# Performance work log

Measured on AMD Instinct MI355X. Metric: run time of the kernel, lower is better.

Reference implementation:

```python
import jax, jax.numpy as jnp
import numpy as np
from jax.experimental import sparse as jsparse

N_ITEMS = 20000   # item catalog size (S is [N_ITEMS, N_ITEMS])
N_USERS = 2048    # user batch
NNZ = 4_000_000


def setup_inputs() -> dict:
    key = jax.random.key(0)
    k1, k2, k3, k4 = jax.random.split(key, 4)
    X = jax.random.normal(k1, (N_USERS, N_ITEMS), dtype=jnp.float32)
    S_vals = jax.random.normal(k2, (NNZ,), dtype=jnp.float32)
    S_rows = jax.random.randint(k3, (NNZ,), 0, N_ITEMS, dtype=jnp.int32)
    S_cols = jax.random.randint(k4, (NNZ,), 0, N_ITEMS, dtype=jnp.int32)
    return {"X": X, "S_vals": S_vals, "S_rows": S_rows, "S_cols": S_cols}


def reference(X, S_vals, S_rows, S_cols):
    # torch.sparse.mm(S, X.t()).t()  ==  X @ S^T, with S sparse COO.
    indices = jnp.stack([S_rows, S_cols], axis=1)  # [nnz, 2]
    S = jsparse.BCOO((S_vals, indices), shape=(N_ITEMS, N_ITEMS))
    # (S @ X^T)^T -> [n_users, n_items]; duplicate indices sum, matching COO semantics.
    return (S @ X.T).T
```

## Files before the change

kernel.cpp:

```cpp
#include <hip/hip_runtime.h>

#define N_ITEMS 20000
#define N_USERS 2048
#define NNZ     4000000
#define LDP     2112
#define HALF_ITEMS 10000
#define CAP_H   192

typedef float    f32x4 __attribute__((ext_vector_type(4)));
typedef unsigned u32x4 __attribute__((ext_vector_type(4)));

#define OFF_XT     ((size_t)0)
#define OFF_CSRPK  ((size_t)84480000)
#define OFF_CNT    (OFF_CSRPK + 30720000)

static __device__ __forceinline__ unsigned short f2bf(float f) {
  unsigned u = __float_as_uint(f);
  unsigned r = (u + 0x7fffu + ((u >> 16) & 1u)) >> 16;
  return (unsigned short)r;
}

#define NT_BLOCKS (313 * 32)
#define NS_BLOCKS ((NNZ / 4 + 255) / 256)

__global__ __launch_bounds__(256) void prep_kernel(
    const float* __restrict__ X, const float* __restrict__ vals,
    const int* __restrict__ rows, const int* __restrict__ cols,
    unsigned short* __restrict__ XT, int* __restrict__ cnt,
    unsigned* __restrict__ csr_pk) {
  int b = blockIdx.x;
  if (b < NT_BLOCKS) {
    __shared__ float tile[64][65];
    int k0 = (b % 313) * 64;
    int u0 = (b / 313) * 64;
    int lane = threadIdx.x & 63;
    int dq = threadIdx.x >> 6;
    #pragma unroll
    for (int m = 0; m < 16; ++m) {
      int u = u0 + dq + 4 * m;
      int k = k0 + lane;
      float v = 0.f;
      if (k < N_ITEMS) v = X[(size_t)u * N_ITEMS + k];
      tile[lane][dq + 4 * m] = v;
    }
    __syncthreads();
    #pragma unroll
    for (int m = 0; m < 16; ++m) {
      int k = k0 + dq + 4 * m;
      if (k < N_ITEMS)
        XT[(size_t)k * LDP + u0 + lane] = f2bf(tile[dq + 4 * m][lane]);
    }
  } else {
    int i = ((b - NT_BLOCKS) * 256 + threadIdx.x) * 4;
    if (i < NNZ) {
      int4   r4 = *reinterpret_cast<const int4*>(rows + i);
      int4   c4 = *reinterpret_cast<const int4*>(cols + i);
      float4 v4 = *reinterpret_cast<const float4*>(vals + i);
      #pragma unroll
      for (int k = 0; k < 4; ++k) {
        int   r = (k == 0) ? r4.x : (k == 1) ? r4.y : (k == 2) ? r4.z : r4.w;
        int   c = (k == 0) ? c4.x : (k == 1) ? c4.y : (k == 2) ? c4.z : c4.w;
        float v = (k == 0) ? v4.x : (k == 1) ? v4.y : (k == 2) ? v4.z : v4.w;
        int h = (c >= HALF_ITEMS) ? 1 : 0;
        int bin = 2 * r + h;
        int pos = atomicAdd(&cnt[bin], 1);
        if (pos >= CAP_H) pos = CAP_H - 1;
        csr_pk[bin * CAP_H + pos] =
            ((unsigned)(c - h * HALF_ITEMS) << 16) | (unsigned)f2bf(v);
      }
    }
  }
}

__global__ __launch_bounds__(256) void spmm_kernel(
    const int* __restrict__ cnt, const unsigned* __restrict__ csr_pk,
    const unsigned short* __restrict__ xt, float* __restrict__ out,
    int uc, int h) {
  __shared__ float tile[8][132];
  int wg = blockIdx.x;
  int xcd = wg & 7;
  int rb = wg >> 3;
  int u0 = (xcd * 2 + uc) * 128;
  int r0 = rb * 8;
  int lane = threadIdx.x & 63;
  int wave = __builtin_amdgcn_readfirstlane((int)(threadIdx.x >> 6));
  unsigned lane4 = 4 * (unsigned)lane;
  const char* xtb = (const char*)(xt + (size_t)h * HALF_ITEMS * LDP + u0);
  int ul = threadIdx.x >> 1;
  int rhalf = (threadIdx.x & 1) * 4;
  float* op = out + (size_t)(u0 + ul) * N_ITEMS + r0 + rhalf;

#define LOAD8(E, BASE)                                                       \
  { u32x4 q0 = __builtin_nontemporal_load(                                   \
        reinterpret_cast<const u32x4*>(csr_pk + (BASE)));                    \
    u32x4 q1 = __builtin_nontemporal_load(                                   \
        reinterpret_cast<const u32x4*>(csr_pk + (BASE) + 4));                \
    E[0] = q0.x; E[1] = q0.y; E[2] = q0.z; E[3] = q0.w;                      \
    E[4] = q1.x; E[5] = q1.y; E[6] = q1.z; E[7] = q1.w; }
#define GATHER8(G, E)                                                        \
  { _Pragma("unroll")                                                        \
    for (int k = 0; k < 8; ++k)                                              \
      G[k] = *reinterpret_cast<const unsigned*>(                             \
          xtb + ((E[k] >> 16) * (unsigned)(LDP * 2) + lane4)); }
#define FMA8(G, E)                                                           \
  { _Pragma("unroll")                                                        \
    for (int k = 0; k < 8; ++k) {                                            \
      float v  = __uint_as_float(E[k] << 16);                \
      float xl = __uint_as_float(G[k] << 16);                                \
      float xh = __uint_as_float(G[k]);                 \
      if (k & 1) { a2 = fmaf(v, xl, a2); a3 = fmaf(v, xh, a3); }             \
      else       { a0 = fmaf(v, xl, a0); a1 = fmaf(v, xh, a1); }             \
    } }

  if (h) {
    f32x4 i0 = __builtin_nontemporal_load(reinterpret_cast<const f32x4*>(op));
    tile[rhalf + 0][ul] = i0.x; tile[rhalf + 1][ul] = i0.y;
    tile[rhalf + 2][ul] = i0.z; tile[rhalf + 3][ul] = i0.w;
    __syncthreads();
  }

  #pragma unroll 1
  for (int rr = 0; rr < 2; ++rr) {
    int r = r0 + wave * 2 + rr;
    int bin = 2 * r + h;
    int jb = bin * CAP_H;
    int cr = __builtin_amdgcn_readfirstlane(cnt[bin]);
    if (cr > CAP_H) cr = CAP_H;
    int nb = (cr + 7) >> 3;
    float a0 = 0.f, a1 = 0.f, a2 = 0.f, a3 = 0.f;
    if (h) {
      a0 = tile[wave * 2 + rr][2 * lane];
      a1 = tile[wave * 2 + rr][2 * lane + 1];
    }
    if (nb >= 2) {
      unsigned e0[8], e1[8], g0[8], g1[8];
      LOAD8(e0, jb)
      GATHER8(g0, e0)
      LOAD8(e1, jb + 8)
      int b = 0;
      for (; b + 3 < nb; b += 2) {
        GATHER8(g1, e1)
        FMA8(g0, e0)
        LOAD8(e0, jb + (b + 2) * 8)
        GATHER8(g0, e0)
        FMA8(g1, e1)
        LOAD8(e1, jb + (b + 3) * 8)
      }
      GATHER8(g1, e1)
      FMA8(g0, e0)
      if (nb - b == 3) {
        LOAD8(e0, jb + (b + 2) * 8)
        GATHER8(g0, e0)
        FMA8(g1, e1)
        FMA8(g0, e0)
      } else {
        FMA8(g1, e1)
      }
    } else if (nb == 1) {
      unsigned e0[8], g0[8];
      LOAD8(e0, jb)
      GATHER8(g0, e0)
      FMA8(g0, e0)
    }
    tile[wave * 2 + rr][2 * lane]     = a0 + a2;
    tile[wave * 2 + rr][2 * lane + 1] = a1 + a3;
  }
#undef LOAD8
#undef GATHER8
#undef FMA8

  __syncthreads();
  f32x4 o;
  o.x = tile[rhalf + 0][ul]; o.y = tile[rhalf + 1][ul];
  o.z = tile[rhalf + 2][ul]; o.w = tile[rhalf + 3][ul];
  __builtin_nontemporal_store(o, reinterpret_cast<f32x4*>(op));
}

extern "C" void kernel_launch(void* const* d_in, const int* in_sizes, int n_in,
                              void* d_out, int out_size, void* d_ws, size_t ws_size,
                              hipStream_t stream) {
  const float* X      = (const float*)d_in[0];
  const float* S_vals = (const float*)d_in[1];
  const int*   S_rows = (const int*)d_in[2];
  const int*   S_cols = (const int*)d_in[3];
  float* out = (float*)d_out;

  char* ws = (char*)d_ws;
  unsigned short* XT = (unsigned short*)(ws + OFF_XT);
  unsigned* csr_pk   = (unsigned*)(ws + OFF_CSRPK);
  int* cnt           = (int*)(ws + OFF_CNT);

  hipMemsetAsync(cnt, 0, 2 * N_ITEMS * sizeof(int), stream);
  hipMemsetAsync(csr_pk, 0, (size_t)2 * N_ITEMS * CAP_H * sizeof(unsigned), stream);
  prep_kernel<<<NT_BLOCKS + NS_BLOCKS, 256, 0, stream>>>(
      X, S_vals, S_rows, S_cols, XT, cnt, csr_pk);
  for (int p = 0; p < 4; ++p)
    spmm_kernel<<<2500 * 8, 256, 0, stream>>>(cnt, csr_pk, XT, out,
                                              p >> 1, p & 1);
}
```

Baseline: 1.088 ms.

## Split columns into quarters and widen each lane to four users per gather

The column space is now split into four quarter-bins of 5000 items (capacity 128 each) instead of two halves. Each spmm launch covers all 256 users of an XCD slice, with every lane gathering 8 bytes (four bf16 users) and using packed two-wide FMAs, so one set of CSR entries is reused across twice as many users. Partial sums are accumulated into the output at the final store rather than preloaded into shared memory. Transpose and scatter are split into separate kernels, and the scatter no longer vectorises four entries per thread. The trade-offs are a tighter per-bin capacity, where overflowing entries get clamped into the last slot, and a larger memset of the padded CSR buffer.

Measured after the change: 2.754 ms. +153.0%, slower.

```diff
diff --git a/kernel.cpp b/kernel.cpp
--- a/kernel.cpp
+++ b/kernel.cpp
@@ -4,15 +4,17 @@
 #define N_USERS 2048
 #define NNZ     4000000
 #define LDP     2112
-#define HALF_ITEMS 10000
-#define CAP_H   192
+#define QITEMS  5000
+#define CAP_Q   128
 
 typedef float    f32x4 __attribute__((ext_vector_type(4)));
+typedef float    f32x2 __attribute__((ext_vector_type(2)));
 typedef unsigned u32x4 __attribute__((ext_vector_type(4)));
+typedef unsigned u32x2 __attribute__((ext_vector_type(2)));
 
 #define OFF_XT     ((size_t)0)
 #define OFF_CSRPK  ((size_t)84480000)
-#define OFF_CNT    (OFF_CSRPK + 30720000)
+#define OFF_CNT    (OFF_CSRPK + 40960000)
 
 static __device__ __forceinline__ unsigned short f2bf(float f) {
   unsigned u = __float_as_uint(f);
@@ -20,75 +22,59 @@
   return (unsigned short)r;
 }
 
-#define NT_BLOCKS (313 * 32)
-#define NS_BLOCKS ((NNZ / 4 + 255) / 256)
+__global__ __launch_bounds__(256) void transpose_kernel(
+    const float* __restrict__ X, unsigned short* __restrict__ XT) {
+  __shared__ float tile[64][65];
+  int k0 = blockIdx.x * 64;
+  int u0 = blockIdx.y * 64;
+  int lane = threadIdx.x & 63;
+  int dq = threadIdx.x >> 6;
+  #pragma unroll
+  for (int m = 0; m < 16; ++m) {
+    int u = u0 + dq + 4 * m;
+    int k = k0 + lane;
+    float v = 0.f;
+    if (k < N_ITEMS) v = X[(size_t)u * N_ITEMS + k];
+    tile[lane][dq + 4 * m] = v;
+  }
+  __syncthreads();
+  #pragma unroll
+  for (int m = 0; m < 16; ++m) {
+    int k = k0 + dq + 4 * m;
+    if (k < N_ITEMS)
+      XT[(size_t)k * LDP + u0 + lane] = f2bf(tile[dq + 4 * m][lane]);
+  }
+}
 
-__global__ __launch_bounds__(256) void prep_kernel(
-    const float* __restrict__ X, const float* __restrict__ vals,
+__global__ __launch_bounds__(256) void scatter_kernel(
     const int* __restrict__ rows, const int* __restrict__ cols,
-    unsigned short* __restrict__ XT, int* __restrict__ cnt,
+    const float* __restrict__ vals, int* __restrict__ cnt,
     unsigned* __restrict__ csr_pk) {
-  int b = blockIdx.x;
-  if (b < NT_BLOCKS) {
-    __shared__ float tile[64][65];
-    int k0 = (b % 313) * 64;
-    int u0 = (b / 313) * 64;
-    int lane = threadIdx.x & 63;
-    int dq = threadIdx.x >> 6;
-    #pragma unroll
-    for (int m = 0; m < 16; ++m) {
-      int u = u0 + dq + 4 * m;
-      int k = k0 + lane;
-      float v = 0.f;
-      if (k < N_ITEMS) v = X[(size_t)u * N_ITEMS + k];
-      tile[lane][dq + 4 * m] = v;
-    }
-    __syncthreads();
-    #pragma unroll
-    for (int m = 0; m < 16; ++m) {
-      int k = k0 + dq + 4 * m;
-      if (k < N_ITEMS)
-        XT[(size_t)k * LDP + u0 + lane] = f2bf(tile[dq + 4 * m][lane]);
-    }
-  } else {
-    int i = ((b - NT_BLOCKS) * 256 + threadIdx.x) * 4;
-    if (i < NNZ) {
-      int4   r4 = *reinterpret_cast<const int4*>(rows + i);
-      int4   c4 = *reinterpret_cast<const int4*>(cols + i);
-      float4 v4 = *reinterpret_cast<const float4*>(vals + i);
-      #pragma unroll
-      for (int k = 0; k < 4; ++k) {
-        int   r = (k == 0) ? r4.x : (k == 1) ? r4.y : (k == 2) ? r4.z : r4.w;
-        int   c = (k == 0) ? c4.x : (k == 1) ? c4.y : (k == 2) ? c4.z : c4.w;
-        float v = (k == 0) ? v4.x : (k == 1) ? v4.y : (k == 2) ? v4.z : v4.w;
-        int h = (c >= HALF_ITEMS) ? 1 : 0;
-        int bin = 2 * r + h;
-        int pos = atomicAdd(&cnt[bin], 1);
-        if (pos >= CAP_H) pos = CAP_H - 1;
-        csr_pk[bin * CAP_H + pos] =
-            ((unsigned)(c - h * HALF_ITEMS) << 16) | (unsigned)f2bf(v);
-      }
-    }
-  }
+  int i = blockIdx.x * 256 + threadIdx.x;
+  int r = rows[i];
+  int c = cols[i];
+  float v = vals[i];
+  int q = c / QITEMS;
+  int cl = c - q * QITEMS;
+  int bin = (r << 2) + q;
+  int pos = atomicAdd(&cnt[bin], 1);
+  if (pos >= CAP_Q) pos = CAP_Q - 1;
+  csr_pk[(bin << 7) + pos] = ((unsigned)cl << 16) | (unsigned)f2bf(v);
 }
 
 __global__ __launch_bounds__(256) void spmm_kernel(
     const int* __restrict__ cnt, const unsigned* __restrict__ csr_pk,
-    const unsigned short* __restrict__ xt, float* __restrict__ out,
-    int uc, int h) {
-  __shared__ float tile[8][132];
+    const unsigned short* __restrict__ xt, float* __restrict__ out, int q) {
+  __shared__ float tile[8][260];
   int wg = blockIdx.x;
   int xcd = wg & 7;
   int rb = wg >> 3;
-  int u0 = (xcd * 2 + uc) * 128;
+  int u0 = xcd * 256;
   int r0 = rb * 8;
   int lane = threadIdx.x & 63;
   int wave = __builtin_amdgcn_readfirstlane((int)(threadIdx.x >> 6));
-  unsigned lane4 = 4 * (unsigned)lane;
-  const char* xtb = (const char*)(xt + (size_t)h * HALF_ITEMS * LDP + u0);
-  int ul = threadIdx.x >> 1;
-  int rhalf = (threadIdx.x & 1) * 4;
-  float* op = out + (size_t)(u0 + ul) * N_ITEMS + r0 + rhalf;
+  unsigned lane8 = 8 * (unsigned)lane;
+  const char* xtb = (const char*)(xt + u0) + (size_t)q * QITEMS * (LDP * 2);
 
 #define LOAD8(E, BASE)                                                       \
   { u32x4 q0 = __builtin_nontemporal_load(                                   \
@@ -100,40 +86,35 @@
 #define GATHER8(G, E)                                                        \
   { _Pragma("unroll")                                                        \
     for (int k = 0; k < 8; ++k)                                              \
-      G[k] = *reinterpret_cast<const unsigned*>(                             \
-          xtb + ((E[k] >> 16) * (unsigned)(LDP * 2) + lane4)); }
+      G[k] = *reinterpret_cast<const u32x2*>(                                \
+          xtb + ((E[k] >> 16) * (unsigned)(LDP * 2) + lane8)); }
 #define FMA8(G, E)                                                           \
   { _Pragma("unroll")                                                        \
     for (int k = 0; k < 8; ++k) {                                            \
-      float v  = __uint_as_float(E[k] << 16);                \
-      float xl = __uint_as_float(G[k] << 16);                                \
-      float xh = __uint_as_float(G[k]);                 \
-      if (k & 1) { a2 = fmaf(v, xl, a2); a3 = fmaf(v, xh, a3); }             \
-      else       { a0 = fmaf(v, xl, a0); a1 = fmaf(v, xh, a1); }             \
+      float vv = __uint_as_float(E[k] << 16);                \
+      f32x2 v2; v2.x = vv; v2.y = vv;                                        \
+      f32x2 x01, x23;                                                        \
+      x01.x = __uint_as_float(G[k].x << 16);                                 \
+      x01.y = __uint_as_float(G[k].x);                  \
+      x23.x = __uint_as_float(G[k].y << 16);                                 \
+      x23.y = __uint_as_float(G[k].y);                  \
+      a01 = __builtin_elementwise_fma(v2, x01, a01);                         \
+      a23 = __builtin_elementwise_fma(v2, x23, a23);                         \
     } }
-
-  if (h) {
-    f32x4 i0 = __builtin_nontemporal_load(reinterpret_cast<const f32x4*>(op));
-    tile[rhalf + 0][ul] = i0.x; tile[rhalf + 1][ul] = i0.y;
-    tile[rhalf + 2][ul] = i0.z; tile[rhalf + 3][ul] = i0.w;
-    __syncthreads();
-  }
 
   #pragma unroll 1
   for (int rr = 0; rr < 2; ++rr) {
     int r = r0 + wave * 2 + rr;
-    int bin = 2 * r + h;
-    int jb = bin * CAP_H;
+    int bin = (r << 2) + q;
+    int jb = bin << 7;
     int cr = __builtin_amdgcn_readfirstlane(cnt[bin]);
-    if (cr > CAP_H) cr = CAP_H;
+    if (cr > CAP_Q) cr = CAP_Q;
     int nb = (cr + 7) >> 3;
-    float a0 = 0.f, a1 = 0.f, a2 = 0.f, a3 = 0.f;
-    if (h) {
-      a0 = tile[wave * 2 + rr][2 * lane];
-      a1 = tile[wave * 2 + rr][2 * lane + 1];
-    }
+    f32x2 a01, a23;
+    a01.x = 0.f; a01.y = 0.f; a23.x = 0.f; a23.y = 0.f;
     if (nb >= 2) {
-      unsigned e0[8], e1[8], g0[8], g1[8];
+      unsigned e0[8], e1[8];
+      u32x2 g0[8], g1[8];
       LOAD8(e0, jb)
       GATHER8(g0, e0)
       LOAD8(e1, jb + 8)
@@ -157,23 +138,34 @@
         FMA8(g1, e1)
       }
     } else if (nb == 1) {
-      unsigned e0[8], g0[8];
+      unsigned e0[8];
+      u32x2 g0[8];
       LOAD8(e0, jb)
       GATHER8(g0, e0)
       FMA8(g0, e0)
     }
-    tile[wave * 2 + rr][2 * lane]     = a0 + a2;
-    tile[wave * 2 + rr][2 * lane + 1] = a1 + a3;
+    f32x4 o;
+    o.x = a01.x; o.y = a01.y; o.z = a23.x; o.w = a23.y;
+    *reinterpret_cast<f32x4*>(&tile[wave * 2 + rr][4 * lane]) = o;
   }
 #undef LOAD8
 #undef GATHER8
 #undef FMA8
 
   __syncthreads();
-  f32x4 o;
-  o.x = tile[rhalf + 0][ul]; o.y = tile[rhalf + 1][ul];
-  o.z = tile[rhalf + 2][ul]; o.w = tile[rhalf + 3][ul];
-  __builtin_nontemporal_store(o, reinterpret_cast<f32x4*>(op));
+  int t = threadIdx.x;
+  float* op = out + (size_t)(u0 + t) * N_ITEMS + r0;
+  f32x4 o0, o1;
+  o0.x = tile[0][t]; o0.y = tile[1][t]; o0.z = tile[2][t]; o0.w = tile[3][t];
+  o1.x = tile[4][t]; o1.y = tile[5][t]; o1.z = tile[6][t]; o1.w = tile[7][t];
+  if (q) {
+    f32x4 i0 = __builtin_nontemporal_load(reinterpret_cast<const f32x4*>(op));
+    f32x4 i1 = __builtin_nontemporal_load(reinterpret_cast<const f32x4*>(op) + 1);
+    o0 += i0;
+    o1 += i1;
+  }
+  __builtin_nontemporal_store(o0, reinterpret_cast<f32x4*>(op));
+  __builtin_nontemporal_store(o1, reinterpret_cast<f32x4*>(op) + 1);
 }
 
 extern "C" void kernel_launch(void* const* d_in, const int* in_sizes, int n_in,
@@ -190,11 +182,10 @@
   unsigned* csr_pk   = (unsigned*)(ws + OFF_CSRPK);
   int* cnt           = (int*)(ws + OFF_CNT);
 
-  hipMemsetAsync(cnt, 0, 2 * N_ITEMS * sizeof(int), stream);
-  hipMemsetAsync(csr_pk, 0, (size_t)2 * N_ITEMS * CAP_H * sizeof(unsigned), stream);
-  prep_kernel<<<NT_BLOCKS + NS_BLOCKS, 256, 0, stream>>>(
-      X, S_vals, S_rows, S_cols, XT, cnt, csr_pk);
-  for (int p = 0; p < 4; ++p)
-    spmm_kernel<<<2500 * 8, 256, 0, stream>>>(cnt, csr_pk, XT, out,
-                                              p >> 1, p & 1);
+  hipMemsetAsync(cnt, 0, 4 * N_ITEMS * sizeof(int), stream);
+  hipMemsetAsync(csr_pk, 0, (size_t)4 * N_ITEMS * CAP_Q * sizeof(unsigned), stream);
+  transpose_kernel<<<dim3(313, 32), 256, 0, stream>>>(X, XT);
+  scatter_kernel<<<NNZ / 256, 256, 0, stream>>>(S_rows, S_cols, S_vals, cnt, csr_pk);
+  for (int q = 0; q < 4; ++q)
+    spmm_kernel<<<2500 * 8, 256, 0, stream>>>(cnt, csr_pk, XT, out, q);
 }
```

## Split prep into transpose and scatter kernels; deepen SpMM gather pipeline to three stages

Applied to the files above, without the earlier changes.

The fused prep kernel is split into a separate transpose kernel and a scalar scatter kernel that handles one nonzero per thread instead of four. The SpMM inner loop now keeps three batches of 8 gathers in flight instead of two, so more memory latency is hidden per wave. The deeper pipeline costs more registers, which may lower occupancy. Splitting prep adds a kernel launch and removes the overlap between the transpose and the scatter.

New measurement: 1.040 ms. -4.5%, faster.

```diff
diff --git a/kernel.cpp b/kernel.cpp
--- a/kernel.cpp
+++ b/kernel.cpp
@@ -20,56 +20,44 @@
   return (unsigned short)r;
 }
 
-#define NT_BLOCKS (313 * 32)
-#define NS_BLOCKS ((NNZ / 4 + 255) / 256)
-
-__global__ __launch_bounds__(256) void prep_kernel(
-    const float* __restrict__ X, const float* __restrict__ vals,
+__global__ __launch_bounds__(256) void transpose_kernel(
+    const float* __restrict__ X, unsigned short* __restrict__ XT) {
+  __shared__ float tile[64][65];
+  int k0 = blockIdx.x * 64;
+  int u0 = blockIdx.y * 64;
+  int lane = threadIdx.x & 63;
+  int dq = threadIdx.x >> 6;
+  #pragma unroll
+  for (int m = 0; m < 16; ++m) {
+    int u = u0 + dq + 4 * m;
+    int k = k0 + lane;
+    float v = 0.f;
+    if (k < N_ITEMS) v = X[(size_t)u * N_ITEMS + k];
+    tile[lane][dq + 4 * m] = v;
+  }
+  __syncthreads();
+  #pragma unroll
+  for (int m = 0; m < 16; ++m) {
+    int k = k0 + dq + 4 * m;
+    if (k < N_ITEMS)
+      XT[(size_t)k * LDP + u0 + lane] = f2bf(tile[dq + 4 * m][lane]);
+  }
+}
+
+__global__ __launch_bounds__(256) void scatter_kernel(
     const int* __restrict__ rows, const int* __restrict__ cols,
-    unsigned short* __restrict__ XT, int* __restrict__ cnt,
+    const float* __restrict__ vals, int* __restrict__ cnt,
     unsigned* __restrict__ csr_pk) {
-  int b = blockIdx.x;
-  if (b < NT_BLOCKS) {
-    __shared__ float tile[64][65];
-    int k0 = (b % 313) * 64;
-    int u0 = (b / 313) * 64;
-    int lane = threadIdx.x & 63;
-    int dq = threadIdx.x >> 6;
-    #pragma unroll
-    for (int m = 0; m < 16; ++m) {
-      int u = u0 + dq + 4 * m;
-      int k = k0 + lane;
-      float v = 0.f;
-      if (k < N_ITEMS) v = X[(size_t)u * N_ITEMS + k];
-      tile[lane][dq + 4 * m] = v;
-    }
-    __syncthreads();
-    #pragma unroll
-    for (int m = 0; m < 16; ++m) {
-      int k = k0 + dq + 4 * m;
-      if (k < N_ITEMS)
-        XT[(size_t)k * LDP + u0 + lane] = f2bf(tile[dq + 4 * m][lane]);
-    }
-  } else {
-    int i = ((b - NT_BLOCKS) * 256 + threadIdx.x) * 4;
-    if (i < NNZ) {
-      int4   r4 = *reinterpret_cast<const int4*>(rows + i);
-      int4   c4 = *reinterpret_cast<const int4*>(cols + i);
-      float4 v4 = *reinterpret_cast<const float4*>(vals + i);
-      #pragma unroll
-      for (int k = 0; k < 4; ++k) {
-        int   r = (k == 0) ? r4.x : (k == 1) ? r4.y : (k == 2) ? r4.z : r4.w;
-        int   c = (k == 0) ? c4.x : (k == 1) ? c4.y : (k == 2) ? c4.z : c4.w;
-        float v = (k == 0) ? v4.x : (k == 1) ? v4.y : (k == 2) ? v4.z : v4.w;
-        int h = (c >= HALF_ITEMS) ? 1 : 0;
-        int bin = 2 * r + h;
-        int pos = atomicAdd(&cnt[bin], 1);
-        if (pos >= CAP_H) pos = CAP_H - 1;
-        csr_pk[bin * CAP_H + pos] =
-            ((unsigned)(c - h * HALF_ITEMS) << 16) | (unsigned)f2bf(v);
-      }
-    }
-  }
+  int i = blockIdx.x * 256 + threadIdx.x;
+  int r = rows[i];
+  int c = cols[i];
+  float v = vals[i];
+  int h = (c >= HALF_ITEMS) ? 1 : 0;
+  int bin = 2 * r + h;
+  int pos = atomicAdd(&cnt[bin], 1);
+  if (pos >= CAP_H) pos = CAP_H - 1;
+  csr_pk[bin * CAP_H + pos] =
+      ((unsigned)(c - h * HALF_ITEMS) << 16) | (unsigned)f2bf(v);
 }
 
 __global__ __launch_bounds__(256) void spmm_kernel(
@@ -132,30 +120,55 @@
       a0 = tile[wave * 2 + rr][2 * lane];
       a1 = tile[wave * 2 + rr][2 * lane + 1];
     }
-    if (nb >= 2) {
+    if (nb >= 3) {
+      unsigned e0[8], e1[8], e2[8], g0[8], g1[8], g2[8];
+      LOAD8(e0, jb)
+      GATHER8(g0, e0)
+      LOAD8(e1, jb + 8)
+      GATHER8(g1, e1)
+      LOAD8(e2, jb + 16)
+      int b = 0;
+      for (; b + 5 < nb; b += 3) {
+        GATHER8(g2, e2)
+        FMA8(g0, e0)
+        LOAD8(e0, jb + (b + 3) * 8)
+        GATHER8(g0, e0)
+        FMA8(g1, e1)
+        LOAD8(e1, jb + (b + 4) * 8)
+        GATHER8(g1, e1)
+        FMA8(g2, e2)
+        LOAD8(e2, jb + (b + 5) * 8)
+      }
+      int m = nb - b;
+      GATHER8(g2, e2)
+      FMA8(g0, e0)
+      if (m == 3) {
+        FMA8(g1, e1)
+        FMA8(g2, e2)
+      } else if (m == 4) {
+        LOAD8(e0, jb + (b + 3) * 8)
+        GATHER8(g0, e0)
+        FMA8(g1, e1)
+        FMA8(g2, e2)
+        FMA8(g0, e0)
+      } else {
+        LOAD8(e0, jb + (b + 3) * 8)
+        GATHER8(g0, e0)
+        FMA8(g1, e1)
+        LOAD8(e1, jb + (b + 4) * 8)
+        GATHER8(g1, e1)
+        FMA8(g2, e2)
+        FMA8(g0, e0)
+        FMA8(g1, e1)
+      }
+    } else if (nb == 2) {
       unsigned e0[8], e1[8], g0[8], g1[8];
       LOAD8(e0, jb)
       GATHER8(g0, e0)
       LOAD8(e1, jb + 8)
-      int b = 0;
-      for (; b + 3 < nb; b += 2) {
-        GATHER8(g1, e1)
-        FMA8(g0, e0)
-        LOAD8(e0, jb + (b + 2) * 8)
-        GATHER8(g0, e0)
-        FMA8(g1, e1)
-        LOAD8(e1, jb + (b + 3) * 8)
-      }
       GATHER8(g1, e1)
       FMA8(g0, e0)
-      if (nb - b == 3) {
-        LOAD8(e0, jb + (b + 2) * 8)
-        GATHER8(g0, e0)
-        FMA8(g1, e1)
-        FMA8(g0, e0)
-      } else {
-        FMA8(g1, e1)
-      }
+      FMA8(g1, e1)
     } else if (nb == 1) {
       unsigned e0[8], g0[8];
       LOAD8(e0, jb)
@@ -192,8 +205,8 @@
 
   hipMemsetAsync(cnt, 0, 2 * N_ITEMS * sizeof(int), stream);
   hipMemsetAsync(csr_pk, 0, (size_t)2 * N_ITEMS * CAP_H * sizeof(unsigned), stream);
-  prep_kernel<<<NT_BLOCKS + NS_BLOCKS, 256, 0, stream>>>(
-      X, S_vals, S_rows, S_cols, XT, cnt, csr_pk);
+  transpose_kernel<<<dim3(313, 32), 256, 0, stream>>>(X, XT);
+  scatter_kernel<<<NNZ / 256, 256, 0, stream>>>(S_rows, S_cols, S_vals, cnt, csr_pk);
   for (int p = 0; p < 4; ++p)
     spmm_kernel<<<2500 * 8, 256, 0, stream>>>(cnt, csr_pk, XT, out,
                                               p >> 1, p & 1);
```
